# Kernel tuning notes

Hardware: AMD Instinct MI355X
Metric: run time of the kernel (lower is better)

Reference implementation:

```python
import jax, jax.numpy as jnp
import numpy as np

T = 1.0  # temperature

def _free_energy(v, W, b, c):
    # v: [B, V]; W: [V, H]; b: [V]; c: [H]
    vW = v @ W                                  # [B, H]
    W_colsum = W.sum(axis=0)                    # [H]
    negF_normal = (v * b).sum(-1) - jax.nn.softplus(vW + c).sum(-1)
    negF_flip = ((1.0 - v) * b).sum(-1) - jax.nn.softplus(W_colsum - vW + c).sum(-1)
    negF = jnp.stack([negF_normal, negF_flip], axis=-1)  # [B, 2]
    return -T * jax.nn.logsumexp(negF / T, axis=-1)      # [B]

def _gibbs_chain(v0, W, b, c, key, k):
    B = v0.shape[0]
    key, k0 = jax.random.split(key)
    u0 = jax.random.bernoulli(k0, 0.5, (B, 1)).astype(v0.dtype)
    b_sum = b.sum()

    def step(carry, _):
        v, u, key = carry
        key, k1, k2, k3 = jax.random.split(key, 4)
        v_branch = u * v + (1.0 - u) * (1.0 - v)
        h = jax.random.bernoulli(k1, jax.nn.sigmoid(v_branch @ W + c)).astype(v.dtype)  # [B,H]
        a = h @ W.T                                                                     # [B,V]
        vb = (v * b).sum(-1)
        va = (v * a).sum(-1)
        dE = -b_sum - a.sum(-1) + 2.0 * vb + 2.0 * va
        u_new = jax.random.bernoulli(k2, jax.nn.sigmoid(dE)).astype(v.dtype)[:, None]
        v_new = jax.random.bernoulli(k3, jax.nn.sigmoid(a + b)).astype(v.dtype)
        v = u_new * v_new + (1.0 - u_new) * (1.0 - v_new)
        return (v, u_new, key), None

    (v_model, _, _), _ = jax.lax.scan(step, (v0, u0, key), None, length=k)
    return v_model

def setup_inputs() -> dict:
    key = jax.random.key(0)
    kv, kw = jax.random.split(key)
    B, V, H = 8192, 1024, 1024
    v_data = jnp.round(jax.random.uniform(kv, (B, V), dtype=jnp.float32))  # binary 0/1
    W = 0.01 * jax.random.normal(kw, (V, H), dtype=jnp.float32)
    b = jnp.zeros((V,), dtype=jnp.float32)
    c = jnp.zeros((H,), dtype=jnp.float32)
    return {"v_data": v_data, "W": W, "b": b, "c": c, "seed": 0}

def reference(v_data, W, b, c, seed):
    K = 10  # Gibbs steps
    key = jax.random.key(seed)
    v_model = _gibbs_chain(v_data, W, b, c, key, K)
    v_model = jax.lax.stop_gradient(v_model)  # .detach() in torch
    loss = _free_energy(v_data, W, b, c).mean() - _free_energy(v_model, W, b, c).mean()
    return loss
```

## Files before the change

kernel.cpp:

```cpp
#include <hip/hip_runtime.h>
#include <hip/hip_bf16.h>
#include <stdint.h>
#include <math.h>


static constexpr int Bn = 8192;
static constexpr int Vn = 1024;
static constexpr int Hn = 1024;
static constexpr int KSTEPS = 10;

typedef _Float16 f16;
typedef f16   f16x4 __attribute__((ext_vector_type(4)));
typedef f16   f16x8 __attribute__((ext_vector_type(8)));
typedef float f32x4 __attribute__((ext_vector_type(4)));

#define GLOBAL_LOAD_LDS16(g, l)                                              \
  __builtin_amdgcn_global_load_lds(                                          \
      (const __attribute__((address_space(1))) uint32_t*)(g),                \
      (__attribute__((address_space(3))) uint32_t*)(l), 16, 0, 0)

__device__ __forceinline__ uint32_t rotl32(uint32_t x, int d) {
  return __builtin_amdgcn_alignbit(x, x, 32 - d);
}

__device__ __forceinline__ void tf2x32(uint32_t k0, uint32_t k1,
                                       uint32_t x0, uint32_t x1,
                                       uint32_t& o0, uint32_t& o1) {
  uint32_t k2 = k0 ^ k1 ^ 0x1BD11BDAu;
#define TFR(r) { x0 += x1; x1 = rotl32(x1, (r)); x1 ^= x0; }
  x0 += k0; x1 += k1;
  TFR(13) TFR(15) TFR(26) TFR(6)
  x0 += k1; x1 += k2 + 1u;
  TFR(17) TFR(29) TFR(16) TFR(24)
  x0 += k2; x1 += k0 + 2u;
  TFR(13) TFR(15) TFR(26) TFR(6)
  x0 += k0; x1 += k1 + 3u;
  TFR(17) TFR(29) TFR(16) TFR(24)
  x0 += k1; x1 += k2 + 4u;
  TFR(13) TFR(15) TFR(26) TFR(6)
  x0 += k2; x1 += k0 + 5u;
#undef TFR
  o0 = x0; o1 = x1;
}

__device__ __forceinline__ float rng_u01(uint2 key, uint32_t idx) {
  uint32_t o0, o1;
  tf2x32(key.x, key.y, 0u, idx, o0, o1);
  uint32_t bits = o0 ^ o1;
  return __uint_as_float((bits >> 9) | 0x3F800000u) - 1.0f;
}

__device__ __attribute__((noinline)) float2 rng2_u01(uint2 key, uint32_t i0,
                                                     uint32_t i1) {
  float2 r;
  r.x = rng_u01(key, i0);
  r.y = rng_u01(key, i1);
  return r;
}

__device__ __forceinline__ float bern_fast(float z, float r01) {
  float e = __expf(-z);
  return (__builtin_fmaf(r01, e, r01) < 1.0f) ? 1.f : 0.f;
}
__device__ __forceinline__ float softplus_fast(float x) {
  return fmaxf(x, 0.f) + __logf(1.f + __expf(-fabsf(x)));
}

template <int CTRL>
__device__ __forceinline__ float dpp_add16(float v) {
  int x = __builtin_amdgcn_update_dpp(0, __float_as_int(v), CTRL, 0xF, 0xF, true);
  return v + __int_as_float(x);
}
__device__ __forceinline__ float red16(float v) {
  v = dpp_add16<0xB1>(v);
  v = dpp_add16<0x4E>(v);
  v = dpp_add16<0x141>(v);
  v = dpp_add16<0x140>(v);
  return v;
}

__global__ void prep_keys(const int* __restrict__ seedp, uint2* __restrict__ keys) {
  if (threadIdx.x != 0 || blockIdx.x != 0) return;
  uint32_t seed = (uint32_t)(*seedp);
  uint2 key = make_uint2(0u, seed);
  uint2 nk, kk;
  tf2x32(key.x, key.y, 0u, 0u, nk.x, nk.y);
  tf2x32(key.x, key.y, 0u, 1u, kk.x, kk.y);
  keys[0] = kk;
  key = nk;
  for (int s = 0; s < KSTEPS; ++s) {
    uint2 t0, t1, t2, t3;
    tf2x32(key.x, key.y, 0u, 0u, t0.x, t0.y);
    tf2x32(key.x, key.y, 0u, 1u, t1.x, t1.y);
    tf2x32(key.x, key.y, 0u, 2u, t2.x, t2.y);
    tf2x32(key.x, key.y, 0u, 3u, t3.x, t3.y);
    key = t0;
    keys[1 + 3*s] = t1;
    keys[2 + 3*s] = t2;
    keys[3 + 3*s] = t3;
  }
}

__global__ __launch_bounds__(256) void colsum_part(
    const float* __restrict__ W, float* __restrict__ part) {
  const int bx = blockIdx.x, t = threadIdx.x;
  float s0 = 0.f, s1 = 0.f, s2 = 0.f, s3 = 0.f;
#pragma unroll
  for (int r = 0; r < 16; ++r) {
    const float* row = W + (size_t)(bx * 16 + r) * Hn;
    s0 += row[t]; s1 += row[t + 256]; s2 += row[t + 512]; s3 += row[t + 768];
  }
  float* p = part + (size_t)bx * Hn;
  p[t] = s0; p[t + 256] = s1; p[t + 512] = s2; p[t + 768] = s3;
}

__global__ __launch_bounds__(256) void colsum_red(
    const float* __restrict__ part, float* __restrict__ cs) {
  const int col = blockIdx.x * 256 + threadIdx.x;
  float s = 0.f;
#pragma unroll
  for (int k = 0; k < 64; ++k) s += part[(size_t)k * Hn + col];
  cs[col] = s;
}

__global__ void bsum_k(const float* __restrict__ bvec, float* __restrict__ bs) {
  __shared__ float sb[4];
  float s = 0.f;
  for (int i = threadIdx.x; i < Vn; i += 256) s += bvec[i];
  for (int off = 32; off > 0; off >>= 1) s += __shfl_down(s, off, 64);
  int wv = threadIdx.x >> 6, ln = threadIdx.x & 63;
  if (ln == 0) sb[wv] = s;
  __syncthreads();
  if (threadIdx.x == 0) bs[0] = sb[0] + sb[1] + sb[2] + sb[3];
}

__global__ __launch_bounds__(256) void cast_W(
    const float* __restrict__ W, f16* __restrict__ Wf, f16* __restrict__ WTf) {
  __shared__ f16 tile[64][65];
  const int j0 = blockIdx.x * 64, i0 = blockIdx.y * 64;
  const int tx = threadIdx.x & 63, tg = threadIdx.x >> 6;
#pragma unroll 4
  for (int rr = 0; rr < 16; ++rr) {
    const int row = tg * 16 + rr;
    float w = W[(size_t)(i0 + row) * Hn + j0 + tx];
    f16 hw = (f16)w;
    Wf[(size_t)(i0 + row) * Hn + j0 + tx] = hw;
    tile[row][tx] = hw;
  }
  __syncthreads();
#pragma unroll 4
  for (int rr = 0; rr < 16; ++rr) {
    const int row = tg * 16 + rr;
    WTf[(size_t)(j0 + row) * Vn + i0 + tx] = tile[tx][row];
  }
}

__global__ void u0_init(const uint2* __restrict__ keys, float* __restrict__ u0) {
  int b = blockIdx.x * 256 + threadIdx.x;
  float r01 = rng_u01(keys[0], (uint32_t)b);
  u0[b] = (r01 < 0.5f) ? 1.f : 0.f;
}

__global__ __launch_bounds__(256) void cast_vx(
    const float* __restrict__ vd, const float* __restrict__ u0,
    const float* __restrict__ bvec, f16* __restrict__ x,
    float* __restrict__ pXB0) {
  const int row = blockIdx.x;
  const int t = threadIdx.x;
  const float uo = u0[row];
  const float4 d  = ((const float4*)(vd + (size_t)row * Vn))[t];
  const float4 bv = ((const float4*)bvec)[t];
  float xv[4] = { d.x, d.y, d.z, d.w };
  if (uo <= 0.5f) { xv[0]=1.f-xv[0]; xv[1]=1.f-xv[1]; xv[2]=1.f-xv[2]; xv[3]=1.f-xv[3]; }
  f16x4 o = { (f16)xv[0], (f16)xv[1], (f16)xv[2], (f16)xv[3] };
  *(f16x4*)(x + (size_t)row * Vn + t * 4) = o;
  float xb = xv[0]*bv.x + xv[1]*bv.y + xv[2]*bv.z + xv[3]*bv.w;
#pragma unroll
  for (int m = 1; m < 8; m <<= 1) xb += __shfl_xor(xb, m, 64);
  if ((t & 7) == 0) pXB0[(size_t)row * 32 + (t >> 3)] = xb;
}

template <int EPI>
__global__ __launch_bounds__(256, 4) void gemm_s(
    const f16* __restrict__ A, const f16* __restrict__ Bm,
    f16* __restrict__ outH, f16* __restrict__ xnew,
    const float* __restrict__ bvec, const float* __restrict__ cvec,
    const float* __restrict__ colsum,
    float* __restrict__ pA, float* __restrict__ pXA, float* __restrict__ pXBn,
    float* __restrict__ pSA, float* __restrict__ pSB,
    const uint2* __restrict__ keys, int keyIdx)
{
  constexpr int N = 1024, K = 1024, BK = 64;
  __shared__ alignas(16) f16 As[128 * BK];
  __shared__ alignas(16) f16 Bs[64 * BK];

  const int t = threadIdx.x, wave = t >> 6, lane = t & 63;
  const int l15 = lane & 15, quad = lane >> 4;
  const int m0 = blockIdx.x * 128, n0 = blockIdx.y * 64;
  const int wm = (wave >> 1) * 64, wn = (wave & 1) * 32;

  const int rbase = lane >> 3;
  const int gch   = (lane & 7) ^ rbase;
  const f16* gA = A  + (size_t)(m0 + wave * 32 + rbase) * K + gch * 8;
  const f16* gB = Bm + (size_t)(n0 + wave * 16 + rbase) * K + gch * 8;
  f16* lA = As + wave * 32 * BK;
  f16* lB = Bs + wave * 16 * BK;

  const int swz = l15 & 7;
  const int oA  = (wm + l15) * BK;
  const int oB  = (wn + l15) * BK;

  uint2 key = make_uint2(0u, 0u);
  if constexpr (EPI != 4) key = keys[keyIdx];

  f32x4 acc[4][2] = {};
  float r01v[32];

#pragma unroll
  for (int ki = 0; ki < 16; ++ki) {
    const int k0 = ki * 64;
#pragma unroll
    for (int i = 0; i < 4; ++i)
      GLOBAL_LOAD_LDS16(gA + k0 + i * 8 * K, lA + i * 8 * BK);
#pragma unroll
    for (int i = 0; i < 2; ++i)
      GLOBAL_LOAD_LDS16(gB + k0 + i * 8 * K, lB + i * 8 * BK);
    if constexpr (EPI != 4) {
      uint32_t idx[2];
#pragma unroll
      for (int j = 0; j < 2; ++j) {
        const int e  = ki * 2 + j;
        const int mt = e >> 3, r = (e >> 1) & 3, nt = e & 1;
        const int gm = m0 + wm + mt * 16 + quad * 4 + r;
        const int gn = n0 + wn + nt * 16 + l15;
        idx[j] = (uint32_t)(gm * N + gn);
      }
      float2 rv = rng2_u01(key, idx[0], idx[1]);
      r01v[ki * 2 + 0] = rv.x;
      r01v[ki * 2 + 1] = rv.y;
    }
    __syncthreads();
#pragma unroll
    for (int kc = 0; kc < 2; ++kc) {
      const int fc = ((kc * 4 + quad) ^ swz) * 8;
      f16x8 af[4], bf[2];
#pragma unroll
      for (int i = 0; i < 4; ++i)
        af[i] = *(const f16x8*)(&As[oA + i * 16 * BK + fc]);
#pragma unroll
      for (int i = 0; i < 2; ++i)
        bf[i] = *(const f16x8*)(&Bs[oB + i * 16 * BK + fc]);
#pragma unroll
      for (int mt = 0; mt < 4; ++mt)
#pragma unroll
        for (int nt = 0; nt < 2; ++nt)
          acc[mt][nt] = __builtin_amdgcn_mfma_f32_16x16x32_f16(af[mt], bf[nt], acc[mt][nt], 0, 0, 0);
    }
    if (ki < 15) __syncthreads();
  }

  const int slot = blockIdx.y * 2 + (wave & 1);

  if constexpr (EPI == 1 || EPI == 2) {
    float csv[2], cvv[2];
#pragma unroll
    for (int nt = 0; nt < 2; ++nt) {
      const int gn = n0 + wn + nt * 16 + l15;
      csv[nt] = colsum[gn];
      cvv[nt] = cvec[gn];
    }
#pragma unroll
    for (int mt = 0; mt < 4; ++mt)
#pragma unroll
      for (int r = 0; r < 4; ++r) {
        const int gm = m0 + wm + mt * 16 + quad * 4 + r;
        float pa = 0.f, pxa = 0.f, sa = 0.f, sb = 0.f;
#pragma unroll
        for (int nt = 0; nt < 2; ++nt) {
          const int gn = n0 + wn + nt * 16 + l15;
          const float val = acc[mt][nt][r];
          const float r01 = r01v[mt * 8 + r * 2 + nt];
          float hq  = bern_fast(val + cvv[nt], r01);
          outH[(size_t)gm * N + gn] = (f16)hq;
          pa  += hq * csv[nt];
          pxa += hq * val;
          if constexpr (EPI == 2) {
            sa += softplus_fast(val + cvv[nt]);
            sb += softplus_fast(csv[nt] - val + cvv[nt]);
          }
        }
        pa  = red16(pa);
        pxa = red16(pxa);
        if constexpr (EPI == 2) {
          sa = red16(sa);
          sb = red16(sb);
        }
        if (l15 == 0) {
          pA [(size_t)gm * 32 + slot] = pa;
          pXA[(size_t)gm * 32 + slot] = pxa;
          if constexpr (EPI == 2) {
            pSA[(size_t)gm * 32 + slot] = sa;
            pSB[(size_t)gm * 32 + slot] = sb;
          }
        }
      }
  } else if constexpr (EPI == 3) {
    float bb[2];
#pragma unroll
    for (int nt = 0; nt < 2; ++nt) bb[nt] = bvec[n0 + wn + nt * 16 + l15];
#pragma unroll
    for (int mt = 0; mt < 4; ++mt)
#pragma unroll
      for (int r = 0; r < 4; ++r) {
        const int gm = m0 + wm + mt * 16 + quad * 4 + r;
        float pxb = 0.f;
#pragma unroll
        for (int nt = 0; nt < 2; ++nt) {
          const int gn = n0 + wn + nt * 16 + l15;
          const float aval = acc[mt][nt][r];
          const float r01 = r01v[mt * 8 + r * 2 + nt];
          float xq  = bern_fast(aval + bb[nt], r01);
          xnew[(size_t)gm * N + gn] = (f16)xq;
          pxb += xq * bb[nt];
        }
        pxb = red16(pxb);
        if (l15 == 0) pXBn[(size_t)gm * 32 + slot] = pxb;
      }
  } else {
    float csv[2], cvv[2];
#pragma unroll
    for (int nt = 0; nt < 2; ++nt) {
      const int gn = n0 + wn + nt * 16 + l15;
      csv[nt] = colsum[gn];
      cvv[nt] = cvec[gn];
    }
#pragma unroll
    for (int mt = 0; mt < 4; ++mt)
#pragma unroll
      for (int r = 0; r < 4; ++r) {
        const int gm = m0 + wm + mt * 16 + quad * 4 + r;
        float sa = 0.f, sb = 0.f;
#pragma unroll
        for (int nt = 0; nt < 2; ++nt) {
          const float val = acc[mt][nt][r];
          sa += softplus_fast(val + cvv[nt]);
          sb += softplus_fast(csv[nt] - val + cvv[nt]);
        }
        sa = red16(sa);
        sb = red16(sb);
        if (l15 == 0) {
          pSA[(size_t)gm * 32 + slot] = sa;
          pSB[(size_t)gm * 32 + slot] = sb;
        }
      }
  }
}

__global__ __launch_bounds__(256) void u_chain(
    const float* __restrict__ pA, const float* __restrict__ pXA,
    const float* __restrict__ pXB, const float* __restrict__ bsum,
    const uint2* __restrict__ keys, const float* __restrict__ u0,
    float* __restrict__ uF)
{
  const int t = threadIdx.x, wave = t >> 6, lane = t & 63;
  const int r2 = lane >> 5, slot = lane & 31;
  const int row = blockIdx.x * 8 + wave * 2 + r2;
  const float bs = bsum[0];
  float uo = u0[row];
  for (int s = 0; s < KSTEPS; ++s) {
    const size_t o = (size_t)s * 32 * Bn + (size_t)row * 32 + slot;
    float sa  = pA [o];
    float sxa = pXA[o];
    float sxb = pXB[o];
#pragma unroll
    for (int m = 1; m < 32; m <<= 1) {
      sa  += __shfl_xor(sa,  m, 64);
      sxa += __shfl_xor(sxa, m, 64);
      sxb += __shfl_xor(sxb, m, 64);
    }
    const float va = (uo > 0.5f) ? sxa : sa - sxa;
    const float vb = (uo > 0.5f) ? sxb : bs - sxb;
    const float dE = -bs - sa + 2.f * vb + 2.f * va;
    uo = bern_fast(dE, rng_u01(keys[2 + 3 * s], (uint32_t)row));
  }
  if (slot == 0) uF[row] = uo;
}

__device__ __forceinline__ float fe_eval(float SA, float SB, float xb,
                                         float uo, float bs) {
  float S1 = (uo > 0.5f) ? SA : SB;
  float S2 = (uo > 0.5f) ? SB : SA;
  float vb = (uo > 0.5f) ? xb : bs - xb;
  float negn = vb - S1;
  float negf = (bs - vb) - S2;
  float mx = fmaxf(negn, negf);
  return -(mx + logf(expf(negn - mx) + expf(negf - mx)));
}

__global__ __launch_bounds__(256) void fe_finish(
    const float* __restrict__ SA0, const float* __restrict__ SB0,
    const float* __restrict__ xb0,
    const float* __restrict__ SAF, const float* __restrict__ SBF,
    const float* __restrict__ xbF,
    const float* __restrict__ u0, const float* __restrict__ uF,
    const float* __restrict__ bsum,
    float* __restrict__ Fd, float* __restrict__ Fm)
{
  const int t = threadIdx.x, wave = t >> 6, lane = t & 63;
  const int r2 = lane >> 5, slot = lane & 31;
  const int row = blockIdx.x * 8 + wave * 2 + r2;
  const size_t o = (size_t)row * 32 + slot;
  const float bs = bsum[0];
  float a0 = SA0[o], b0 = SB0[o], x0 = xb0[o];
  float aF = SAF[o], bF = SBF[o], xF = xbF[o];
#pragma unroll
  for (int m = 1; m < 32; m <<= 1) {
    a0 += __shfl_xor(a0, m, 64);  b0 += __shfl_xor(b0, m, 64);
    x0 += __shfl_xor(x0, m, 64);  aF += __shfl_xor(aF, m, 64);
    bF += __shfl_xor(bF, m, 64);  xF += __shfl_xor(xF, m, 64);
  }
  if (slot == 0) {
    Fd[row] = fe_eval(a0, b0, x0, u0[row], bs);
    Fm[row] = fe_eval(aF, bF, xF, uF[row], bs);
  }
}

__global__ __launch_bounds__(256) void finalize_k(
    const float* __restrict__ Fd, const float* __restrict__ Fm, float* __restrict__ out)
{
  __shared__ double sb[8];
  double sd = 0.0, sm = 0.0;
  for (int i = threadIdx.x; i < Bn; i += 256) { sd += (double)Fd[i]; sm += (double)Fm[i]; }
  for (int off = 32; off > 0; off >>= 1) { sd += __shfl_down(sd, off, 64); sm += __shfl_down(sm, off, 64); }
  const int wv = threadIdx.x >> 6, ln = threadIdx.x & 63;
  if (ln == 0) { sb[wv] = sd; sb[4 + wv] = sm; }
  __syncthreads();
  if (threadIdx.x == 0) {
    sd = sb[0] + sb[1] + sb[2] + sb[3];
    sm = sb[4] + sb[5] + sb[6] + sb[7];
    out[0] = (float)((sd - sm) / (double)Bn);
  }
}

extern "C" void kernel_launch(void* const* d_in, const int* in_sizes, int n_in,
                              void* d_out, int out_size, void* d_ws, size_t ws_size,
                              hipStream_t stream) {
  const float* v_data = (const float*)d_in[0];
  const float* W      = (const float*)d_in[1];
  const float* bvec   = (const float*)d_in[2];
  const float* cvec   = (const float*)d_in[3];
  const int*   seedp  = (const int*)d_in[4];
  float* out = (float*)d_out;

  char* ws = (char*)d_ws;
  size_t off = 0;
  auto alloc = [&](size_t bytes) -> void* {
    void* p = ws + off;
    off += (bytes + 255) & ~(size_t)255;
    return p;
  };
  f16*   xb0  = (f16*)alloc((size_t)Bn * Vn * 2);
  f16*   xb1  = (f16*)alloc((size_t)Bn * Vn * 2);
  f16*   h    = (f16*)alloc((size_t)Bn * Hn * 2);
  f16*   Wf   = (f16*)alloc((size_t)Vn * Hn * 2);
  f16*   WTf  = (f16*)alloc((size_t)Vn * Hn * 2);
  float* cpart  = (float*)alloc(64 * Hn * 4);
  float* colsum = (float*)alloc(Hn * 4);
  float* bsum   = (float*)alloc(256);
  uint2* keys   = (uint2*)alloc(64 * sizeof(uint2));
  float* u0     = (float*)alloc(Bn * 4);
  float* uF     = (float*)alloc(Bn * 4);
  float* pA     = (float*)alloc((size_t)KSTEPS * 32 * Bn * 4);
  float* pXA    = (float*)alloc((size_t)KSTEPS * 32 * Bn * 4);
  float* pXB    = (float*)alloc((size_t)(KSTEPS + 1) * 32 * Bn * 4);
  float* SA0    = (float*)alloc((size_t)32 * Bn * 4);
  float* SB0    = (float*)alloc((size_t)32 * Bn * 4);
  float* SAF    = (float*)alloc((size_t)32 * Bn * 4);
  float* SBF    = (float*)alloc((size_t)32 * Bn * 4);
  float* Fd     = (float*)alloc(Bn * 4);
  float* Fm     = (float*)alloc(Bn * 4);
  (void)ws_size; (void)in_sizes; (void)n_in; (void)out_size;

  prep_keys<<<1, 64, 0, stream>>>(seedp, keys);
  colsum_part<<<64, 256, 0, stream>>>(W, cpart);
  colsum_red<<<4, 256, 0, stream>>>(cpart, colsum);
  bsum_k<<<1, 256, 0, stream>>>(bvec, bsum);
  cast_W<<<dim3(Hn / 64, Vn / 64), 256, 0, stream>>>(W, Wf, WTf);
  u0_init<<<Bn / 256, 256, 0, stream>>>(keys, u0);
  cast_vx<<<Bn, 256, 0, stream>>>(v_data, u0, bvec, xb0, pXB);

  dim3 gg(Bn / 128, Hn / 64);
  f16* xs[2] = { xb0, xb1 };
  const size_t SL = (size_t)32 * Bn;

  for (int s = 0; s < KSTEPS; ++s) {
    if (s == 0) {
      gemm_s<2><<<gg, 256, 0, stream>>>(xs[0], WTf, h, nullptr, nullptr, cvec,
                                        colsum, pA, pXA, nullptr, SA0, SB0,
                                        keys, 1);
    } else {
      gemm_s<1><<<gg, 256, 0, stream>>>(xs[s & 1], WTf, h, nullptr, nullptr, cvec,
                                        colsum, pA + (size_t)s * SL,
                                        pXA + (size_t)s * SL, nullptr,
                                        nullptr, nullptr, keys, 1 + 3 * s);
    }
    gemm_s<3><<<gg, 256, 0, stream>>>(h, Wf, nullptr, xs[(s + 1) & 1], bvec,
                                      nullptr, nullptr, nullptr, nullptr,
                                      pXB + (size_t)(s + 1) * SL,
                                      nullptr, nullptr, keys, 3 + 3 * s);
  }

  gemm_s<4><<<gg, 256, 0, stream>>>(xs[KSTEPS & 1], WTf, nullptr, nullptr,
                                    nullptr, cvec, colsum, nullptr, nullptr,
                                    nullptr, SAF, SBF, keys, 0);

  u_chain<<<Bn / 8, 256, 0, stream>>>(pA, pXA, pXB, bsum, keys, u0, uF);
  fe_finish<<<Bn / 8, 256, 0, stream>>>(SA0, SB0, pXB,
                                        SAF, SBF, pXB + (size_t)KSTEPS * SL,
                                        u0, uF, bsum, Fd, Fm);
  finalize_k<<<1, 256, 0, stream>>>(Fd, Fm, out);
}
```

Before: 856.3 us.

## Double-buffer LDS with prefetch and enlarge GEMM tile to 128x128 with 512 threads

Each GEMM block now computes a 128x128 output tile with eight waves instead of a 128x64 tile with four. The K loop uses two LDS buffers: the next two K-slices are loaded ahead, and each buffer is refilled by global-to-LDS loads after its second-half fragments are read. Explicit waitcnt and barriers replace the two full __syncthreads per iteration, so memory loads overlap with MFMA work, and each block reuses the A tile across twice as many columns. In exchange each block uses twice the LDS (64 KB), which limits how many blocks fit on a CU. The grid also drops to 512 blocks, which may leave some CUs less well filled.

```diff
diff --git a/kernel.cpp b/kernel.cpp
--- a/kernel.cpp
+++ b/kernel.cpp
@@ -181,7 +181,7 @@
 }
 
 template <int EPI>
-__global__ __launch_bounds__(256, 4) void gemm_s(
+__global__ __launch_bounds__(512, 4) void gemm_s(
     const f16* __restrict__ A, const f16* __restrict__ Bm,
     f16* __restrict__ outH, f16* __restrict__ xnew,
     const float* __restrict__ bvec, const float* __restrict__ cvec,
@@ -191,20 +191,19 @@
     const uint2* __restrict__ keys, int keyIdx)
 {
   constexpr int N = 1024, K = 1024, BK = 64;
-  __shared__ alignas(16) f16 As[128 * BK];
-  __shared__ alignas(16) f16 Bs[64 * BK];
+  __shared__ alignas(16) f16 As[2][128 * BK];
+  __shared__ alignas(16) f16 Bs[2][128 * BK];
 
   const int t = threadIdx.x, wave = t >> 6, lane = t & 63;
   const int l15 = lane & 15, quad = lane >> 4;
-  const int m0 = blockIdx.x * 128, n0 = blockIdx.y * 64;
-  const int wm = (wave >> 1) * 64, wn = (wave & 1) * 32;
+  const int m0 = blockIdx.x * 128, n0 = blockIdx.y * 128;
+  const int wm = (wave >> 2) * 64, wn = (wave & 3) * 32;
 
   const int rbase = lane >> 3;
   const int gch   = (lane & 7) ^ rbase;
-  const f16* gA = A  + (size_t)(m0 + wave * 32 + rbase) * K + gch * 8;
+  const f16* gA = A  + (size_t)(m0 + wave * 16 + rbase) * K + gch * 8;
   const f16* gB = Bm + (size_t)(n0 + wave * 16 + rbase) * K + gch * 8;
-  f16* lA = As + wave * 32 * BK;
-  f16* lB = Bs + wave * 16 * BK;
+  const int woff = wave * 16 * BK;
 
   const int swz = l15 & 7;
   const int oA  = (wm + l15) * BK;
@@ -217,14 +216,31 @@
   float r01v[32];
 
 #pragma unroll
+  for (int i = 0; i < 2; ++i) {
+    GLOBAL_LOAD_LDS16(gA + i * 8 * K,      As[0] + woff + i * 8 * BK);
+    GLOBAL_LOAD_LDS16(gB + i * 8 * K,      Bs[0] + woff + i * 8 * BK);
+  }
+#pragma unroll
+  for (int i = 0; i < 2; ++i) {
+    GLOBAL_LOAD_LDS16(gA + 64 + i * 8 * K, As[1] + woff + i * 8 * BK);
+    GLOBAL_LOAD_LDS16(gB + 64 + i * 8 * K, Bs[1] + woff + i * 8 * BK);
+  }
+  asm volatile("s_waitcnt vmcnt(4)" ::: "memory");
+  __builtin_amdgcn_s_barrier();
+
+#pragma unroll
   for (int ki = 0; ki < 16; ++ki) {
-    const int k0 = ki * 64;
-#pragma unroll
-    for (int i = 0; i < 4; ++i)
-      GLOBAL_LOAD_LDS16(gA + k0 + i * 8 * K, lA + i * 8 * BK);
-#pragma unroll
-    for (int i = 0; i < 2; ++i)
-      GLOBAL_LOAD_LDS16(gB + k0 + i * 8 * K, lB + i * 8 * BK);
+    const int cur = ki & 1;
+    const f16* rA = As[cur];
+    const f16* rB = Bs[cur];
+    f16x8 a0[4], b0[2];
+    {
+      const int fc = (quad ^ swz) * 8;
+#pragma unroll
+      for (int i = 0; i < 4; ++i) a0[i] = *(const f16x8*)(&rA[oA + i * 16 * BK + fc]);
+#pragma unroll
+      for (int i = 0; i < 2; ++i) b0[i] = *(const f16x8*)(&rB[oB + i * 16 * BK + fc]);
+    }
     if constexpr (EPI != 4) {
       uint32_t idx[2];
 #pragma unroll
@@ -239,27 +255,44 @@
       r01v[ki * 2 + 0] = rv.x;
       r01v[ki * 2 + 1] = rv.y;
     }
-    __syncthreads();
-#pragma unroll
-    for (int kc = 0; kc < 2; ++kc) {
-      const int fc = ((kc * 4 + quad) ^ swz) * 8;
-      f16x8 af[4], bf[2];
-#pragma unroll
-      for (int i = 0; i < 4; ++i)
-        af[i] = *(const f16x8*)(&As[oA + i * 16 * BK + fc]);
-#pragma unroll
-      for (int i = 0; i < 2; ++i)
-        bf[i] = *(const f16x8*)(&Bs[oB + i * 16 * BK + fc]);
-#pragma unroll
-      for (int mt = 0; mt < 4; ++mt)
-#pragma unroll
-        for (int nt = 0; nt < 2; ++nt)
-          acc[mt][nt] = __builtin_amdgcn_mfma_f32_16x16x32_f16(af[mt], bf[nt], acc[mt][nt], 0, 0, 0);
-    }
-    if (ki < 15) __syncthreads();
-  }
-
-  const int slot = blockIdx.y * 2 + (wave & 1);
+#pragma unroll
+    for (int mt = 0; mt < 4; ++mt)
+#pragma unroll
+      for (int nt = 0; nt < 2; ++nt)
+        acc[mt][nt] = __builtin_amdgcn_mfma_f32_16x16x32_f16(a0[mt], b0[nt], acc[mt][nt], 0, 0, 0);
+    f16x8 a1[4], b1[2];
+    {
+      const int fc = ((4 + quad) ^ swz) * 8;
+#pragma unroll
+      for (int i = 0; i < 4; ++i) a1[i] = *(const f16x8*)(&rA[oA + i * 16 * BK + fc]);
+#pragma unroll
+      for (int i = 0; i < 2; ++i) b1[i] = *(const f16x8*)(&rB[oB + i * 16 * BK + fc]);
+    }
+    if (ki < 14) {
+      asm volatile("s_waitcnt lgkmcnt(0)" ::: "memory");
+      __builtin_amdgcn_s_barrier();
+      const int kt = (ki + 2) * 64;
+#pragma unroll
+      for (int i = 0; i < 2; ++i) {
+        GLOBAL_LOAD_LDS16(gA + kt + i * 8 * K, (f16*)As[cur] + woff + i * 8 * BK);
+        GLOBAL_LOAD_LDS16(gB + kt + i * 8 * K, (f16*)Bs[cur] + woff + i * 8 * BK);
+      }
+    }
+#pragma unroll
+    for (int mt = 0; mt < 4; ++mt)
+#pragma unroll
+      for (int nt = 0; nt < 2; ++nt)
+        acc[mt][nt] = __builtin_amdgcn_mfma_f32_16x16x32_f16(a1[mt], b1[nt], acc[mt][nt], 0, 0, 0);
+    if (ki < 14) {
+      asm volatile("s_waitcnt vmcnt(4)" ::: "memory");
+      __builtin_amdgcn_s_barrier();
+    } else if (ki == 14) {
+      asm volatile("s_waitcnt vmcnt(0)" ::: "memory");
+      __builtin_amdgcn_s_barrier();
+    }
+  }
+
+  const int slot = blockIdx.y * 4 + (wave & 3);
 
   if constexpr (EPI == 1 || EPI == 2) {
     float csv[2], cvv[2];
@@ -489,28 +522,28 @@
   u0_init<<<Bn / 256, 256, 0, stream>>>(keys, u0);
   cast_vx<<<Bn, 256, 0, stream>>>(v_data, u0, bvec, xb0, pXB);
 
-  dim3 gg(Bn / 128, Hn / 64);
+  dim3 gg(Bn / 128, Hn / 128);
   f16* xs[2] = { xb0, xb1 };
   const size_t SL = (size_t)32 * Bn;
 
   for (int s = 0; s < KSTEPS; ++s) {
     if (s == 0) {
-      gemm_s<2><<<gg, 256, 0, stream>>>(xs[0], WTf, h, nullptr, nullptr, cvec,
+      gemm_s<2><<<gg, 512, 0, stream>>>(xs[0], WTf, h, nullptr, nullptr, cvec,
                                         colsum, pA, pXA, nullptr, SA0, SB0,
                                         keys, 1);
     } else {
-      gemm_s<1><<<gg, 256, 0, stream>>>(xs[s & 1], WTf, h, nullptr, nullptr, cvec,
+      gemm_s<1><<<gg, 512, 0, stream>>>(xs[s & 1], WTf, h, nullptr, nullptr, cvec,
                                         colsum, pA + (size_t)s * SL,
                                         pXA + (size_t)s * SL, nullptr,
                                         nullptr, nullptr, keys, 1 + 3 * s);
     }
-    gemm_s<3><<<gg, 256, 0, stream>>>(h, Wf, nullptr, xs[(s + 1) & 1], bvec,
+    gemm_s<3><<<gg, 512, 0, stream>>>(h, Wf, nullptr, xs[(s + 1) & 1], bvec,
                                       nullptr, nullptr, nullptr, nullptr,
                                       pXB + (size_t)(s + 1) * SL,
                                       nullptr, nullptr, keys, 3 + 3 * s);
   }
 
-  gemm_s<4><<<gg, 256, 0, stream>>>(xs[KSTEPS & 1], WTf, nullptr, nullptr,
+  gemm_s<4><<<gg, 512, 0, stream>>>(xs[KSTEPS & 1], WTf, nullptr, nullptr,
                                     nullptr, cvec, colsum, nullptr, nullptr,
                                     nullptr, SAF, SBF, keys, 0);
 
```

After: 909.6 us. 6.2% more time.
